# Kernel optimization log

Hardware: AMD Instinct MI355X
Metric: run time of the kernel (lower is better)

The kernel has to match this reference:

```python
import jax, jax.numpy as jnp
from jax import lax
import numpy as np

B, H, W, C = 4, 128, 128, 128   # C == d_route == n_heads, patch_len == H
OFFSET_RANGE = 5.0              # offset_range_factor == kernel == 5
SCALE = C ** -0.5               # self.scale_factor = d_route**-0.5
CYCLE = 168


def grid_sample_bilinear(img, grid):
    """torch.nn.functional.grid_sample(mode='bilinear', padding_mode='zeros', align_corners=False).
    img: (B,C,H,W); grid: (B,H,W,2) with (x,y) in [-1,1]."""
    Bn, Cn, Hn, Wn = img.shape
    xg = (grid[..., 0] + 1.0) * (Wn / 2.0) - 0.5
    yg = (grid[..., 1] + 1.0) * (Hn / 2.0) - 0.5
    x0 = jnp.floor(xg)
    y0 = jnp.floor(yg)
    img_flat = img.reshape(Bn, Cn, Hn * Wn)
    out = jnp.zeros_like(img)
    for xi in (x0, x0 + 1.0):
        for yi in (y0, y0 + 1.0):
            wgt = (1.0 - jnp.abs(xg - xi)) * (1.0 - jnp.abs(yg - yi))
            valid = (xi >= 0) & (xi <= Wn - 1) & (yi >= 0) & (yi <= Hn - 1)
            ix = jnp.clip(xi, 0, Wn - 1).astype(jnp.int32)
            iy = jnp.clip(yi, 0, Hn - 1).astype(jnp.int32)
            idx = (iy * Wn + ix).reshape(Bn, 1, -1)                      # (B,1,H*W)
            vals = jnp.take_along_axis(img_flat, idx, axis=2).reshape(Bn, Cn, Hn, Wn)
            out = out + vals * (wgt * valid.astype(img.dtype))[:, None, :, :]
    return out


def setup_inputs():
    key = jax.random.key(0)
    ks = jax.random.split(key, 12)
    s = C ** -0.5
    inp = {
        "x": jax.random.normal(ks[0], (B, H, W, C), dtype=jnp.float32),
        "cycle_index": jax.random.randint(ks[1], (B, 128), 0, CYCLE),  # dead path in cycle_mode='None'
        "Wq": jax.random.normal(ks[2], (C, C), dtype=jnp.float32) * s,
        "bq": jnp.zeros((C,), dtype=jnp.float32),
        "Wk": jax.random.normal(ks[3], (C, C), dtype=jnp.float32) * s,
        "bk": jnp.zeros((C,), dtype=jnp.float32),
        "Wv": jax.random.normal(ks[4], (C, C), dtype=jnp.float32) * s,
        "bv": jnp.zeros((C,), dtype=jnp.float32),
        "Wo": jax.random.normal(ks[5], (C, C), dtype=jnp.float32) * s,
        "bo": jnp.zeros((C,), dtype=jnp.float32),
        "Wc1": jax.random.normal(ks[6], (C, C, 5, 5), dtype=jnp.float32) * (1.0 / np.sqrt(C * 25)),
        "bc1": jnp.zeros((C,), dtype=jnp.float32),
        "Wc2": jax.random.normal(ks[7], (2, C), dtype=jnp.float32) * s,   # 1x1 conv, no bias
        "rel_bias": jax.random.normal(ks[8], (1, C, H, 1), dtype=jnp.float32) * 0.02,
    }
    return inp


def reference(x, cycle_index, Wq, bq, Wk, bk, Wv, bv, Wo, bo, Wc1, bc1, Wc2, rel_bias):
    Bn, Hn, Wn, Cn = x.shape
    xc = jnp.transpose(x, (0, 3, 1, 2))                                  # (B,C,H,W)
    # proj_q (1x1 conv) on x (cycle_mode='None')
    q = jnp.einsum('oc,bchw->bohw', Wq, xc) + bq[None, :, None, None]
    # proj_offset: 5x5 conv (pad 2) -> 1x1 conv to 2 channels, tanh * offset_range_factor
    c1 = lax.conv_general_dilated(q, Wc1, (1, 1), ((2, 2), (2, 2)),
                                  dimension_numbers=('NCHW', 'OIHW', 'NCHW')) + bc1[None, :, None, None]
    offset = jnp.tanh(jnp.einsum('oc,bchw->bohw', Wc2, c1)) * OFFSET_RANGE  # (B,2,H,W)
    # create_grid_like + normalize_grid (faithful, incl. x-coord normalized by H and vice versa)
    gx, gy = jnp.meshgrid(jnp.arange(Wn, dtype=x.dtype), jnp.arange(Hn, dtype=x.dtype), indexing='xy')
    grid = jnp.stack([gx, gy], axis=0)                                   # (2,H,W)
    vgrid = grid[None] + offset                                          # (B,2,H,W)
    gh = 2.0 * vgrid[:, 0] / max(Hn - 1, 1) - 1.0
    gw = 2.0 * vgrid[:, 1] / max(Wn - 1, 1) - 1.0
    sgrid = jnp.stack([gh, gw], axis=-1)                                 # (B,H,W,2) = (x,y) for grid_sample
    x_sampled = grid_sample_bilinear(xc, sgrid)                          # (B,C,H,W); n_groups=1 -> rearrange is identity
    k = (jnp.einsum('oc,bchw->bohw', Wk, x_sampled) + bk[None, :, None, None]).reshape(Bn * Cn, Hn, Wn)
    v = (jnp.einsum('oc,bchw->bohw', Wv, x_sampled) + bv[None, :, None, None] + rel_bias).reshape(Bn * Cn, Hn, Wn)
    qr = q.reshape(Bn * Cn, Hn, Wn)
    scores = jnp.einsum('bid,bjd->bij', qr, k) * SCALE                   # (B*C,H,H)
    attn = jax.nn.softmax(scores, axis=-1)
    out = jnp.einsum('bij,bjd->bid', attn, v)                            # (B*C,H,W)
    out = out.reshape(Bn, Hn, Wn, Cn)                                    # faithful raw reshape (as in original)
    return out @ Wo.T + bo
```

## Files before the change

kernel.cpp:

```cpp
#include <hip/hip_runtime.h>
#include <math.h>

#define IMG 16384

typedef short short8  __attribute__((ext_vector_type(8)));
typedef float floatx4 __attribute__((ext_vector_type(4)));

__device__ __forceinline__ float4 ld4(const float* p) {
    return *reinterpret_cast<const float4*>(p);
}
__device__ __forceinline__ short f2bf(float f) {
    union { float f; unsigned u; } v; v.f = f;
    unsigned r = v.u + 0x7fffu + ((v.u >> 16) & 1u);
    return (short)(r >> 16);
}
__device__ __forceinline__ float bf2f(short s) {
    union { unsigned u; float f; } v;
    v.u = ((unsigned)(unsigned short)s) << 16;
    return v.f;
}

__launch_bounds__(256)
__global__ void k_wprep(const float* __restrict__ Wc1, const float* __restrict__ Wc2,
                        const float* __restrict__ bc1, const float* __restrict__ Wq,
                        const float* __restrict__ bq,
                        float* __restrict__ W2, float* __restrict__ cst,
                        float* __restrict__ b_eff) {
    __shared__ float U[128];
    __shared__ float red[256];
    __shared__ float wc2[128];
    __shared__ float bql[128];
    const int tt = blockIdx.x;
    const int tch = tt / 25, tap = tt % 25;
    const int t = threadIdx.x;
    if (t < 128) { wc2[t] = Wc2[tch * 128 + t]; bql[t] = bq[t]; }
    __syncthreads();
    const int c = t & 127, half = t >> 7;
    float p = 0.f;
    for (int o = half * 64; o < half * 64 + 64; ++o)
        p += wc2[o] * Wc1[(o * 128 + c) * 25 + tap];
    red[half * 128 + c] = p;
    __syncthreads();
    if (t < 128) U[t] = red[t] + red[128 + t];
    __syncthreads();
    float p2 = 0.f;
    for (int cc = half * 64; cc < half * 64 + 64; ++cc)
        p2 += U[cc] * Wq[cc * 128 + c];
    red[half * 128 + c] = p2;
    __syncthreads();
    if (t < 128) W2[tt * 128 + t] = red[t] + red[128 + t];
    if (t < 128) red[t] = U[t] * bql[t];
    __syncthreads();
    if (t == 0) {
        float s = 0.f;
        for (int j = 0; j < 128; ++j) s += red[j];
        cst[tt] = s;
    }
    if (tap == 0) {
        __syncthreads();
        if (t < 128) red[t] = wc2[t] * bc1[t];
        __syncthreads();
        if (t == 0) {
            float s = 0.f;
            for (int j = 0; j < 128; ++j) s += red[j];
            b_eff[tch] = s;
        }
    }
}

__launch_bounds__(256)
__global__ void k_cvt(const float* __restrict__ x,
                      const float* __restrict__ Wq, const float* __restrict__ Wk,
                      const float* __restrict__ Wv, const float* __restrict__ Wo,
                      short* __restrict__ x_bf, short* __restrict__ wbf) {
    const int gid = blockIdx.x;
    if (gid < 4096) {
        int i = gid * 256 + threadIdx.x;
        const float* p = x + (size_t)i * 8;
        float4 a = ld4(p), b = ld4(p + 4);
        short8 o;
        o[0] = f2bf(a.x); o[1] = f2bf(a.y); o[2] = f2bf(a.z); o[3] = f2bf(a.w);
        o[4] = f2bf(b.x); o[5] = f2bf(b.y); o[6] = f2bf(b.z); o[7] = f2bf(b.w);
        *reinterpret_cast<short8*>(x_bf + (size_t)i * 8) = o;
    } else {
        int i = (gid - 4096) * 256 + threadIdx.x;
        int base = i * 8;
        int sel = base >> 14, off = base & 16383;
        const float* s = (sel == 0) ? Wq : (sel == 1) ? Wk : (sel == 2) ? Wv : Wo;
        float4 a = ld4(s + off), b = ld4(s + off + 4);
        short8 o;
        o[0] = f2bf(a.x); o[1] = f2bf(a.y); o[2] = f2bf(a.z); o[3] = f2bf(a.w);
        o[4] = f2bf(b.x); o[5] = f2bf(b.y); o[6] = f2bf(b.z); o[7] = f2bf(b.w);
        *reinterpret_cast<short8*>(wbf + base) = o;
    }
}

__launch_bounds__(256)
__global__ void k_off(const float* __restrict__ x, const float* __restrict__ W2,
                      const float* __restrict__ cst, float* __restrict__ P) {
    __shared__ float Wlds[128 * 68];
    __shared__ float Alds[32 * 68];
    const int t = threadIdx.x;
    const int pg = t & 15, og = t >> 4;
    const int p0 = blockIdx.x * 64;
    const int b = p0 >> 14, pix0 = p0 & (IMG - 1);

    for (int id = t; id < 128 * 64; id += 256) {
        int k = id >> 6, o = id & 63;
        Wlds[k * 68 + o] = (o < 50) ? W2[o * 128 + k] : 0.f;
    }
    float acc[4][4];
#pragma unroll
    for (int i = 0; i < 4; ++i)
#pragma unroll
        for (int j = 0; j < 4; ++j) acc[i][j] = 0.f;

    for (int kc = 0; kc < 128; kc += 32) {
        __syncthreads();
#pragma unroll
        for (int rep = 0; rep < 2; ++rep) {
            int id = rep * 256 + t;
            int m = id >> 3, k4 = (id & 7) * 4;
            float4 v = ld4(x + (size_t)(p0 + m) * 128 + kc + k4);
            Alds[(k4 + 0) * 68 + m] = v.x;
            Alds[(k4 + 1) * 68 + m] = v.y;
            Alds[(k4 + 2) * 68 + m] = v.z;
            Alds[(k4 + 3) * 68 + m] = v.w;
        }
        __syncthreads();
#pragma unroll
        for (int k = 0; k < 32; ++k) {
            float4 a = *reinterpret_cast<float4*>(&Alds[k * 68 + 4 * pg]);
            float4 wv = *reinterpret_cast<float4*>(&Wlds[(kc + k) * 68 + 4 * og]);
            float av[4] = {a.x, a.y, a.z, a.w};
            float wf[4] = {wv.x, wv.y, wv.z, wv.w};
#pragma unroll
            for (int i = 0; i < 4; ++i)
#pragma unroll
                for (int j = 0; j < 4; ++j)
                    acc[i][j] = fmaf(av[i], wf[j], acc[i][j]);
        }
    }
    __syncthreads();
#pragma unroll
    for (int j = 0; j < 4; ++j) {
        int o = 4 * og + j;
        float c = (o < 50) ? cst[o] : 0.f;
        *reinterpret_cast<float4*>(&Wlds[o * 68 + 4 * pg]) =
            make_float4(acc[0][j] + c, acc[1][j] + c, acc[2][j] + c, acc[3][j] + c);
    }
    __syncthreads();
    for (int id = t; id < 50 * 16; id += 256) {
        int o = id >> 4, px4 = (id & 15) * 4;
        float4 v = *reinterpret_cast<float4*>(&Wlds[o * 68 + px4]);
        *reinterpret_cast<float4*>(P + ((size_t)(b * 50 + o)) * IMG + pix0 + px4) = v;
    }
}

__launch_bounds__(256)
__global__ void k_fused(const float* __restrict__ P, const float* __restrict__ b_eff,
                        const short* __restrict__ x_bf, const short* __restrict__ wbf,
                        const float* __restrict__ bq, const float* __restrict__ bk,
                        const float* __restrict__ bv, const float* __restrict__ rel,
                        short* __restrict__ q_bf, short* __restrict__ k_bf,
                        short* __restrict__ v_bf) {
    __shared__ __align__(16) char smem[70656];
    float* rowsP  = (float*)smem;
    short* xrow   = (short*)smem;
    short* bufS   = (short*)smem;
    short* xsT    = (short*)(smem + 34816);
    float* offs_l = (float*)(smem + 69632);

    const int t = threadIdx.x;
    const int w = t >> 6, l = t & 63, l15 = l & 15, quad = l >> 4;
    const int mh = w >> 1, nh = w & 1;
    const int bh = blockIdx.x;
    const int b = bh >> 7, h = bh & 127;

    for (int id = t; id < 1600; id += 256) {
        int o = id >> 5, q4 = (id & 31) * 4;
        int di = (o % 25) / 5;
        int r = h + di - 2;
        float4 v = make_float4(0.f, 0.f, 0.f, 0.f);
        if (r >= 0 && r < 128)
            v = ld4(P + ((size_t)(b * 50 + o)) * IMG + r * 128 + q4);
        *reinterpret_cast<float4*>(&rowsP[o * 132 + q4]) = v;
    }
    __syncthreads();
    {
        int wp = t & 127, tc = t >> 7;
        float acc = 0.f;
#pragma unroll
        for (int di = 0; di < 5; ++di)
#pragma unroll
            for (int dj = 0; dj < 5; ++dj) {
                int wj = wp + dj - 2;
                if (wj >= 0 && wj < 128)
                    acc += rowsP[(tc * 25 + di * 5 + dj) * 132 + wj];
            }
        offs_l[tc * 128 + wp] = tanhf(acc + b_eff[tc]) * 5.0f;
    }
    __syncthreads();

    for (int id = t; id < 2048; id += 256) {
        int px = id >> 4, c8 = id & 15;
        *reinterpret_cast<short8*>(&xrow[px * 136 + c8 * 8]) =
            *reinterpret_cast<const short8*>(
                x_bf + (((size_t)(b * 128 + h)) * 128 + px) * 128 + c8 * 8);
    }
    for (int id = t; id < 2048; id += 256) {
        int px = id >> 4, c8 = id & 15;
        float ox = offs_l[px];
        float oy = offs_l[128 + px];
        float xg = ((float)px + ox) * (128.0f / 127.0f) - 0.5f;
        float yg = ((float)h  + oy) * (128.0f / 127.0f) - 0.5f;
        float x0f = floorf(xg), y0f = floorf(yg);
        float fx = xg - x0f, fy = yg - y0f;
        int x0 = (int)x0f, y0 = (int)y0f;
        float s[8];
#pragma unroll
        for (int r = 0; r < 8; ++r) s[r] = 0.f;
#pragma unroll
        for (int tap = 0; tap < 4; ++tap) {
            int xi = x0 + (tap & 1), yi = y0 + (tap >> 1);
            float wgt = ((tap & 1) ? fx : 1.f - fx) * ((tap >> 1) ? fy : 1.f - fy);
            if (xi >= 0 && xi < 128 && yi >= 0 && yi < 128) {
                short8 v = *reinterpret_cast<const short8*>(
                    x_bf + (((size_t)(b * 128 + yi)) * 128 + xi) * 128 + c8 * 8);
#pragma unroll
                for (int r = 0; r < 8; ++r) s[r] = fmaf(wgt, bf2f(v[r]), s[r]);
            }
        }
        short8 o;
#pragma unroll
        for (int r = 0; r < 8; ++r) o[r] = f2bf(s[r]);
        *reinterpret_cast<short8*>(&xsT[px * 136 + c8 * 8]) = o;
    }
    __syncthreads();

#pragma unroll
    for (int g = 0; g < 3; ++g) {
        const short* Asrc = (g == 0) ? xrow : xsT;
        const short* Wg   = wbf + g * 16384;
        const float* bias = (g == 0) ? bq : (g == 1) ? bk : bv;
        short* outg       = (g == 0) ? q_bf : (g == 1) ? k_bf : v_bf;

        floatx4 acc[4][4];
#pragma unroll
        for (int im = 0; im < 4; ++im)
#pragma unroll
            for (int in = 0; in < 4; ++in)
                acc[im][in] = (floatx4){0.f, 0.f, 0.f, 0.f};
#pragma unroll
        for (int kc = 0; kc < 128; kc += 32) {
            short8 af[4], bf_[4];
#pragma unroll
            for (int im = 0; im < 4; ++im)
                af[im] = *reinterpret_cast<const short8*>(
                    &Asrc[(mh * 64 + im * 16 + l15) * 136 + kc + quad * 8]);
#pragma unroll
            for (int in = 0; in < 4; ++in)
                bf_[in] = *reinterpret_cast<const short8*>(
                    Wg + (nh * 64 + in * 16 + l15) * 128 + kc + quad * 8);
#pragma unroll
            for (int im = 0; im < 4; ++im)
#pragma unroll
                for (int in = 0; in < 4; ++in)
                    acc[im][in] = __builtin_amdgcn_mfma_f32_16x16x32_bf16(
                        af[im], bf_[in], acc[im][in], 0, 0, 0);
        }
        float bb[4];
#pragma unroll
        for (int in = 0; in < 4; ++in) {
            int o = nh * 64 + in * 16 + l15;
            bb[in] = bias[o] + ((g == 2) ? rel[o * 128 + h] : 0.f);
        }
        __syncthreads();
#pragma unroll
        for (int im = 0; im < 4; ++im)
#pragma unroll
            for (int in = 0; in < 4; ++in) {
                int col = nh * 64 + in * 16 + l15;
#pragma unroll
                for (int r = 0; r < 4; ++r) {
                    int row = mh * 64 + im * 16 + quad * 4 + r;
                    bufS[col * 136 + row] = f2bf(acc[im][in][r] + bb[in]);
                }
            }
        __syncthreads();
        for (int id = t; id < 2048; id += 256) {
            int o = id >> 4, seg = id & 15;
            *reinterpret_cast<short8*>(
                outg + ((size_t)(b * 128 + o)) * IMG + h * 128 + seg * 8)
                = *reinterpret_cast<const short8*>(&bufS[o * 136 + seg * 8]);
        }
        __syncthreads();
    }
}

__launch_bounds__(256)
__global__ void k_attn3(const short* __restrict__ q_bf, const short* __restrict__ k_bf,
                        const short* __restrict__ v_bf, const short* __restrict__ WoB,
                        const float* __restrict__ bo, float* __restrict__ outp) {
    __shared__ __align__(16) short Pb[128 * 136];
    __shared__ __align__(16) short vT[128 * 136];
    __shared__ float redm[2 * 128];
    __shared__ float reds[2 * 128];

    const int t = threadIdx.x;
    const int w = t >> 6, l = t & 63, l15 = l & 15, quad = l >> 4;
    const int mh = w >> 1, nh = w & 1;
    const size_t hb = (size_t)blockIdx.x * IMG;
    const short* qp = q_bf + hb;
    const short* kp = k_bf + hb;
    const short* vp = v_bf + hb;

    for (int id = t; id < 2048; id += 256) {
        int j = id >> 4, seg = id & 15;
        short8 v8 = *reinterpret_cast<const short8*>(vp + j * 128 + seg * 8);
#pragma unroll
        for (int r = 0; r < 8; ++r)
            vT[(seg * 8 + r) * 136 + j] = v8[r];
    }

    floatx4 acc[4][4];
#pragma unroll
    for (int im = 0; im < 4; ++im)
#pragma unroll
        for (int in = 0; in < 4; ++in)
            acc[im][in] = (floatx4){0.f, 0.f, 0.f, 0.f};

#pragma unroll
    for (int kc = 0; kc < 128; kc += 32) {
        short8 af[4], bf_[4];
#pragma unroll
        for (int im = 0; im < 4; ++im)
            af[im] = *reinterpret_cast<const short8*>(
                qp + (mh * 64 + im * 16 + l15) * 128 + kc + quad * 8);
#pragma unroll
        for (int in = 0; in < 4; ++in)
            bf_[in] = *reinterpret_cast<const short8*>(
                kp + (nh * 64 + in * 16 + l15) * 128 + kc + quad * 8);
#pragma unroll
        for (int im = 0; im < 4; ++im)
#pragma unroll
            for (int in = 0; in < 4; ++in)
                acc[im][in] = __builtin_amdgcn_mfma_f32_16x16x32_bf16(
                    af[im], bf_[in], acc[im][in], 0, 0, 0);
    }

    const float scale = 0.08838834764831845f;
    float mloc[4][4];
#pragma unroll
    for (int im = 0; im < 4; ++im)
#pragma unroll
        for (int r = 0; r < 4; ++r) {
            float m = acc[im][0][r];
#pragma unroll
            for (int in = 1; in < 4; ++in) m = fmaxf(m, acc[im][in][r]);
            mloc[im][r] = m;
        }
#pragma unroll
    for (int mask = 1; mask < 16; mask <<= 1)
#pragma unroll
        for (int im = 0; im < 4; ++im)
#pragma unroll
            for (int r = 0; r < 4; ++r)
                mloc[im][r] = fmaxf(mloc[im][r], __shfl_xor(mloc[im][r], mask, 64));
    if (l15 == 0) {
#pragma unroll
        for (int im = 0; im < 4; ++im)
#pragma unroll
            for (int r = 0; r < 4; ++r)
                redm[nh * 128 + mh * 64 + im * 16 + quad * 4 + r] = mloc[im][r];
    }
    __syncthreads();
    float sloc[4][4];
#pragma unroll
    for (int im = 0; im < 4; ++im)
#pragma unroll
        for (int r = 0; r < 4; ++r) {
            int row = mh * 64 + im * 16 + quad * 4 + r;
            float m = fmaxf(redm[row], redm[128 + row]);
            float ss = 0.f;
#pragma unroll
            for (int in = 0; in < 4; ++in) {
                float e = __expf((acc[im][in][r] - m) * scale);
                acc[im][in][r] = e;
                ss += e;
            }
            sloc[im][r] = ss;
        }
#pragma unroll
    for (int mask = 1; mask < 16; mask <<= 1)
#pragma unroll
        for (int im = 0; im < 4; ++im)
#pragma unroll
            for (int r = 0; r < 4; ++r)
                sloc[im][r] += __shfl_xor(sloc[im][r], mask, 64);
    if (l15 == 0) {
#pragma unroll
        for (int im = 0; im < 4; ++im)
#pragma unroll
            for (int r = 0; r < 4; ++r)
                reds[nh * 128 + mh * 64 + im * 16 + quad * 4 + r] = sloc[im][r];
    }
    __syncthreads();
#pragma unroll
    for (int im = 0; im < 4; ++im)
#pragma unroll
        for (int r = 0; r < 4; ++r) {
            int row = mh * 64 + im * 16 + quad * 4 + r;
            float inv = 1.0f / (reds[row] + reds[128 + row]);
#pragma unroll
            for (int in = 0; in < 4; ++in) {
                int col = nh * 64 + in * 16 + l15;
                Pb[row * 136 + col] = f2bf(acc[im][in][r] * inv);
            }
        }
    __syncthreads();

#pragma unroll
    for (int im = 0; im < 4; ++im)
#pragma unroll
        for (int in = 0; in < 4; ++in)
            acc[im][in] = (floatx4){0.f, 0.f, 0.f, 0.f};
#pragma unroll
    for (int kc = 0; kc < 128; kc += 32) {
        short8 af[4], bf_[4];
#pragma unroll
        for (int im = 0; im < 4; ++im)
            af[im] = *reinterpret_cast<const short8*>(
                &Pb[(mh * 64 + im * 16 + l15) * 136 + kc + quad * 8]);
#pragma unroll
        for (int in = 0; in < 4; ++in)
            bf_[in] = *reinterpret_cast<const short8*>(
                &vT[(nh * 64 + in * 16 + l15) * 136 + kc + quad * 8]);
#pragma unroll
        for (int im = 0; im < 4; ++im)
#pragma unroll
            for (int in = 0; in < 4; ++in)
                acc[im][in] = __builtin_amdgcn_mfma_f32_16x16x32_bf16(
                    af[im], bf_[in], acc[im][in], 0, 0, 0);
    }
    __syncthreads();
#pragma unroll
    for (int im = 0; im < 4; ++im)
#pragma unroll
        for (int in = 0; in < 4; ++in) {
            int col = nh * 64 + in * 16 + l15;
#pragma unroll
            for (int r = 0; r < 4; ++r) {
                int row = mh * 64 + im * 16 + quad * 4 + r;
                Pb[row * 136 + col] = f2bf(acc[im][in][r]);
            }
        }
    __syncthreads();

    float bb[4];
#pragma unroll
    for (int in = 0; in < 4; ++in) bb[in] = bo[nh * 64 + in * 16 + l15];
#pragma unroll
    for (int im = 0; im < 4; ++im)
#pragma unroll
        for (int in = 0; in < 4; ++in)
            acc[im][in] = (floatx4){0.f, 0.f, 0.f, 0.f};
#pragma unroll
    for (int kc = 0; kc < 128; kc += 32) {
        short8 af[4], bf_[4];
#pragma unroll
        for (int im = 0; im < 4; ++im)
            af[im] = *reinterpret_cast<const short8*>(
                &Pb[(mh * 64 + im * 16 + l15) * 136 + kc + quad * 8]);
#pragma unroll
        for (int in = 0; in < 4; ++in)
            bf_[in] = *reinterpret_cast<const short8*>(
                WoB + (nh * 64 + in * 16 + l15) * 128 + kc + quad * 8);
#pragma unroll
        for (int im = 0; im < 4; ++im)
#pragma unroll
            for (int in = 0; in < 4; ++in)
                acc[im][in] = __builtin_amdgcn_mfma_f32_16x16x32_bf16(
                    af[im], bf_[in], acc[im][in], 0, 0, 0);
    }
#pragma unroll
    for (int im = 0; im < 4; ++im)
#pragma unroll
        for (int in = 0; in < 4; ++in) {
            int col = nh * 64 + in * 16 + l15;
#pragma unroll
            for (int r = 0; r < 4; ++r) {
                int row = mh * 64 + im * 16 + quad * 4 + r;
                outp[hb + (size_t)row * 128 + col] = acc[im][in][r] + bb[in];
            }
        }
}

extern "C" void kernel_launch(void* const* d_in, const int* in_sizes, int n_in,
                              void* d_out, int out_size, void* d_ws, size_t ws_size,
                              hipStream_t stream) {
    const float* x   = (const float*)d_in[0];
    const float* Wq  = (const float*)d_in[2];
    const float* bq  = (const float*)d_in[3];
    const float* Wk  = (const float*)d_in[4];
    const float* bk  = (const float*)d_in[5];
    const float* Wv  = (const float*)d_in[6];
    const float* bv  = (const float*)d_in[7];
    const float* Wo  = (const float*)d_in[8];
    const float* bo  = (const float*)d_in[9];
    const float* Wc1 = (const float*)d_in[10];
    const float* bc1 = (const float*)d_in[11];
    const float* Wc2 = (const float*)d_in[12];
    const float* rel = (const float*)d_in[13];

    char* wsb = (char*)d_ws;
    short* q_bf  = (short*)(wsb);
    short* k_bf  = (short*)(wsb + 1ull * 16777216);
    short* v_bf  = (short*)(wsb + 2ull * 16777216);
    short* x_bf  = (short*)(wsb + 3ull * 16777216);
    float* P     = (float*)(wsb + 4ull * 16777216);
    float* W2    = (float*)(wsb + 4ull * 16777216 + 13107200);
    float* cst   = W2 + 6400;
    float* b_eff = cst + 64;
    short* wbf   = (short*)(b_eff + 16);
    float* outp  = (float*)d_out;

    hipLaunchKernelGGL(k_cvt,   dim3(4128), dim3(256), 0, stream, x, Wq, Wk, Wv, Wo, x_bf, wbf);
    hipLaunchKernelGGL(k_wprep, dim3(50),   dim3(256), 0, stream, Wc1, Wc2, bc1, Wq, bq, W2, cst, b_eff);
    hipLaunchKernelGGL(k_off,   dim3(1024), dim3(256), 0, stream, x, W2, cst, P);
    hipLaunchKernelGGL(k_fused, dim3(512),  dim3(256), 0, stream, P, b_eff, x_bf, wbf,
                       bq, bk, bv, rel, q_bf, k_bf, v_bf);
    hipLaunchKernelGGL(k_attn3, dim3(512),  dim3(256), 0, stream, q_bf, k_bf, v_bf,
                       wbf + 49152, bo, outp);
}
```

Before: 223.4 us.

## Fold conversion kernel into wprep/offset kernels and restructure QKV projection

Removes the standalone fp32-to-bf16 conversion kernel. Weight conversion now runs in extra blocks of k_wprep, and x conversion happens inside k_off while it already loads x. The fused QKV kernel reads q-projection A operands straight from global x_bf instead of staging a row in LDS. It computes K and V in one pass sharing the sampled A fragments, and stores outputs directly as 4-wide bf16 writes instead of transposing through LDS. LDS is cut so two blocks fit per CU, at the cost of more register pressure and less coalesced global stores.

```diff
diff --git a/kernel.cpp b/kernel.cpp
--- a/kernel.cpp
+++ b/kernel.cpp
@@ -3,6 +3,7 @@
 
 #define IMG 16384
 
+typedef short short4v __attribute__((ext_vector_type(4)));
 typedef short short8  __attribute__((ext_vector_type(8)));
 typedef float floatx4 __attribute__((ext_vector_type(4)));
 
@@ -23,16 +24,29 @@
 __launch_bounds__(256)
 __global__ void k_wprep(const float* __restrict__ Wc1, const float* __restrict__ Wc2,
                         const float* __restrict__ bc1, const float* __restrict__ Wq,
-                        const float* __restrict__ bq,
+                        const float* __restrict__ bq, const float* __restrict__ Wk,
+                        const float* __restrict__ Wv, const float* __restrict__ Wo,
                         float* __restrict__ W2, float* __restrict__ cst,
-                        float* __restrict__ b_eff) {
+                        float* __restrict__ b_eff, short* __restrict__ wbf) {
+    const int t = threadIdx.x;
+    if (blockIdx.x >= 50) {
+        int i = (blockIdx.x - 50) * 256 + t;
+        int base = i * 8;
+        int sel = base >> 14, off = base & 16383;
+        const float* s = (sel == 0) ? Wq : (sel == 1) ? Wk : (sel == 2) ? Wv : Wo;
+        float4 a = ld4(s + off), b = ld4(s + off + 4);
+        short8 o;
+        o[0] = f2bf(a.x); o[1] = f2bf(a.y); o[2] = f2bf(a.z); o[3] = f2bf(a.w);
+        o[4] = f2bf(b.x); o[5] = f2bf(b.y); o[6] = f2bf(b.z); o[7] = f2bf(b.w);
+        *reinterpret_cast<short8*>(wbf + base) = o;
+        return;
+    }
     __shared__ float U[128];
     __shared__ float red[256];
     __shared__ float wc2[128];
     __shared__ float bql[128];
     const int tt = blockIdx.x;
     const int tch = tt / 25, tap = tt % 25;
-    const int t = threadIdx.x;
     if (t < 128) { wc2[t] = Wc2[tch * 128 + t]; bql[t] = bq[t]; }
     __syncthreads();
     const int c = t & 127, half = t >> 7;
@@ -69,35 +83,9 @@
 }
 
 __launch_bounds__(256)
-__global__ void k_cvt(const float* __restrict__ x,
-                      const float* __restrict__ Wq, const float* __restrict__ Wk,
-                      const float* __restrict__ Wv, const float* __restrict__ Wo,
-                      short* __restrict__ x_bf, short* __restrict__ wbf) {
-    const int gid = blockIdx.x;
-    if (gid < 4096) {
-        int i = gid * 256 + threadIdx.x;
-        const float* p = x + (size_t)i * 8;
-        float4 a = ld4(p), b = ld4(p + 4);
-        short8 o;
-        o[0] = f2bf(a.x); o[1] = f2bf(a.y); o[2] = f2bf(a.z); o[3] = f2bf(a.w);
-        o[4] = f2bf(b.x); o[5] = f2bf(b.y); o[6] = f2bf(b.z); o[7] = f2bf(b.w);
-        *reinterpret_cast<short8*>(x_bf + (size_t)i * 8) = o;
-    } else {
-        int i = (gid - 4096) * 256 + threadIdx.x;
-        int base = i * 8;
-        int sel = base >> 14, off = base & 16383;
-        const float* s = (sel == 0) ? Wq : (sel == 1) ? Wk : (sel == 2) ? Wv : Wo;
-        float4 a = ld4(s + off), b = ld4(s + off + 4);
-        short8 o;
-        o[0] = f2bf(a.x); o[1] = f2bf(a.y); o[2] = f2bf(a.z); o[3] = f2bf(a.w);
-        o[4] = f2bf(b.x); o[5] = f2bf(b.y); o[6] = f2bf(b.z); o[7] = f2bf(b.w);
-        *reinterpret_cast<short8*>(wbf + base) = o;
-    }
-}
-
-__launch_bounds__(256)
 __global__ void k_off(const float* __restrict__ x, const float* __restrict__ W2,
-                      const float* __restrict__ cst, float* __restrict__ P) {
+                      const float* __restrict__ cst, float* __restrict__ P,
+                      short* __restrict__ x_bf) {
     __shared__ float Wlds[128 * 68];
     __shared__ float Alds[32 * 68];
     const int t = threadIdx.x;
@@ -126,6 +114,8 @@
             Alds[(k4 + 1) * 68 + m] = v.y;
             Alds[(k4 + 2) * 68 + m] = v.z;
             Alds[(k4 + 3) * 68 + m] = v.w;
+            short4v s = {f2bf(v.x), f2bf(v.y), f2bf(v.z), f2bf(v.w)};
+            *reinterpret_cast<short4v*>(x_bf + (size_t)(p0 + m) * 128 + kc + k4) = s;
         }
         __syncthreads();
 #pragma unroll
@@ -157,19 +147,17 @@
     }
 }
 
-__launch_bounds__(256)
-__global__ void k_fused(const float* __restrict__ P, const float* __restrict__ b_eff,
-                        const short* __restrict__ x_bf, const short* __restrict__ wbf,
-                        const float* __restrict__ bq, const float* __restrict__ bk,
-                        const float* __restrict__ bv, const float* __restrict__ rel,
-                        short* __restrict__ q_bf, short* __restrict__ k_bf,
-                        short* __restrict__ v_bf) {
-    __shared__ __align__(16) char smem[70656];
+__launch_bounds__(256, 2)
+__global__ void k_fused2(const float* __restrict__ P, const float* __restrict__ b_eff,
+                         const short* __restrict__ x_bf, const short* __restrict__ wbf,
+                         const float* __restrict__ bq, const float* __restrict__ bk,
+                         const float* __restrict__ bv, const float* __restrict__ rel,
+                         short* __restrict__ q_bf, short* __restrict__ k_bf,
+                         short* __restrict__ v_bf) {
+    __shared__ __align__(16) char smem[62240];
     float* rowsP  = (float*)smem;
-    short* xrow   = (short*)smem;
-    short* bufS   = (short*)smem;
-    short* xsT    = (short*)(smem + 34816);
-    float* offs_l = (float*)(smem + 69632);
+    short* xsT    = (short*)(smem + 26400);
+    float* offs_l = (float*)(smem + 61216);
 
     const int t = threadIdx.x;
     const int w = t >> 6, l = t & 63, l15 = l & 15, quad = l >> 4;
@@ -202,12 +190,6 @@
     }
     __syncthreads();
 
-    for (int id = t; id < 2048; id += 256) {
-        int px = id >> 4, c8 = id & 15;
-        *reinterpret_cast<short8*>(&xrow[px * 136 + c8 * 8]) =
-            *reinterpret_cast<const short8*>(
-                x_bf + (((size_t)(b * 128 + h)) * 128 + px) * 128 + c8 * 8);
-    }
     for (int id = t; id < 2048; id += 256) {
         int px = id >> 4, c8 = id & 15;
         float ox = offs_l[px];
@@ -236,15 +218,9 @@
         for (int r = 0; r < 8; ++r) o[r] = f2bf(s[r]);
         *reinterpret_cast<short8*>(&xsT[px * 136 + c8 * 8]) = o;
     }
-    __syncthreads();
-
-#pragma unroll
-    for (int g = 0; g < 3; ++g) {
-        const short* Asrc = (g == 0) ? xrow : xsT;
-        const short* Wg   = wbf + g * 16384;
-        const float* bias = (g == 0) ? bq : (g == 1) ? bk : bv;
-        short* outg       = (g == 0) ? q_bf : (g == 1) ? k_bf : v_bf;
-
+
+    {
+        const short* xr = x_bf + ((size_t)(b * 128 + h)) * 128 * 128;
         floatx4 acc[4][4];
 #pragma unroll
         for (int im = 0; im < 4; ++im)
@@ -257,11 +233,11 @@
 #pragma unroll
             for (int im = 0; im < 4; ++im)
                 af[im] = *reinterpret_cast<const short8*>(
-                    &Asrc[(mh * 64 + im * 16 + l15) * 136 + kc + quad * 8]);
+                    xr + (mh * 64 + im * 16 + l15) * 128 + kc + quad * 8);
 #pragma unroll
             for (int in = 0; in < 4; ++in)
                 bf_[in] = *reinterpret_cast<const short8*>(
-                    Wg + (nh * 64 + in * 16 + l15) * 128 + kc + quad * 8);
+                    wbf + (nh * 64 + in * 16 + l15) * 128 + kc + quad * 8);
 #pragma unroll
             for (int im = 0; im < 4; ++im)
 #pragma unroll
@@ -269,32 +245,72 @@
                     acc[im][in] = __builtin_amdgcn_mfma_f32_16x16x32_bf16(
                         af[im], bf_[in], acc[im][in], 0, 0, 0);
         }
-        float bb[4];
 #pragma unroll
         for (int in = 0; in < 4; ++in) {
             int o = nh * 64 + in * 16 + l15;
-            bb[in] = bias[o] + ((g == 2) ? rel[o * 128 + h] : 0.f);
-        }
-        __syncthreads();
+            float bb = bq[o];
+#pragma unroll
+            for (int im = 0; im < 4; ++im) {
+                int px0 = mh * 64 + im * 16 + quad * 4;
+                short4v s = {f2bf(acc[im][in][0] + bb), f2bf(acc[im][in][1] + bb),
+                             f2bf(acc[im][in][2] + bb), f2bf(acc[im][in][3] + bb)};
+                *reinterpret_cast<short4v*>(
+                    q_bf + ((size_t)(b * 128 + o)) * IMG + h * 128 + px0) = s;
+            }
+        }
+    }
+    __syncthreads();
+
+    {
+        floatx4 ak[4][4], av[4][4];
 #pragma unroll
         for (int im = 0; im < 4; ++im)
 #pragma unroll
             for (int in = 0; in < 4; ++in) {
-                int col = nh * 64 + in * 16 + l15;
-#pragma unroll
-                for (int r = 0; r < 4; ++r) {
-                    int row = mh * 64 + im * 16 + quad * 4 + r;
-                    bufS[col * 136 + row] = f2bf(acc[im][in][r] + bb[in]);
+                ak[im][in] = (floatx4){0.f, 0.f, 0.f, 0.f};
+                av[im][in] = (floatx4){0.f, 0.f, 0.f, 0.f};
+            }
+#pragma unroll
+        for (int kc = 0; kc < 128; kc += 32) {
+            short8 af[4], bk_[4], bv_[4];
+#pragma unroll
+            for (int im = 0; im < 4; ++im)
+                af[im] = *reinterpret_cast<const short8*>(
+                    &xsT[(mh * 64 + im * 16 + l15) * 136 + kc + quad * 8]);
+#pragma unroll
+            for (int in = 0; in < 4; ++in) {
+                bk_[in] = *reinterpret_cast<const short8*>(
+                    wbf + 16384 + (nh * 64 + in * 16 + l15) * 128 + kc + quad * 8);
+                bv_[in] = *reinterpret_cast<const short8*>(
+                    wbf + 32768 + (nh * 64 + in * 16 + l15) * 128 + kc + quad * 8);
+            }
+#pragma unroll
+            for (int im = 0; im < 4; ++im)
+#pragma unroll
+                for (int in = 0; in < 4; ++in) {
+                    ak[im][in] = __builtin_amdgcn_mfma_f32_16x16x32_bf16(
+                        af[im], bk_[in], ak[im][in], 0, 0, 0);
+                    av[im][in] = __builtin_amdgcn_mfma_f32_16x16x32_bf16(
+                        af[im], bv_[in], av[im][in], 0, 0, 0);
                 }
-            }
-        __syncthreads();
-        for (int id = t; id < 2048; id += 256) {
-            int o = id >> 4, seg = id & 15;
-            *reinterpret_cast<short8*>(
-                outg + ((size_t)(b * 128 + o)) * IMG + h * 128 + seg * 8)
-                = *reinterpret_cast<const short8*>(&bufS[o * 136 + seg * 8]);
-        }
-        __syncthreads();
+        }
+#pragma unroll
+        for (int in = 0; in < 4; ++in) {
+            int o = nh * 64 + in * 16 + l15;
+            float bbk = bk[o];
+            float bbv = bv[o] + rel[o * 128 + h];
+#pragma unroll
+            for (int im = 0; im < 4; ++im) {
+                int px0 = mh * 64 + im * 16 + quad * 4;
+                size_t base = ((size_t)(b * 128 + o)) * IMG + h * 128 + px0;
+                short4v sk = {f2bf(ak[im][in][0] + bbk), f2bf(ak[im][in][1] + bbk),
+                              f2bf(ak[im][in][2] + bbk), f2bf(ak[im][in][3] + bbk)};
+                short4v sv = {f2bf(av[im][in][0] + bbv), f2bf(av[im][in][1] + bbv),
+                              f2bf(av[im][in][2] + bbv), f2bf(av[im][in][3] + bbv)};
+                *reinterpret_cast<short4v*>(k_bf + base) = sk;
+                *reinterpret_cast<short4v*>(v_bf + base) = sv;
+            }
+        }
     }
 }
 
@@ -525,11 +541,11 @@
     short* wbf   = (short*)(b_eff + 16);
     float* outp  = (float*)d_out;
 
-    hipLaunchKernelGGL(k_cvt,   dim3(4128), dim3(256), 0, stream, x, Wq, Wk, Wv, Wo, x_bf, wbf);
-    hipLaunchKernelGGL(k_wprep, dim3(50),   dim3(256), 0, stream, Wc1, Wc2, bc1, Wq, bq, W2, cst, b_eff);
-    hipLaunchKernelGGL(k_off,   dim3(1024), dim3(256), 0, stream, x, W2, cst, P);
-    hipLaunchKernelGGL(k_fused, dim3(512),  dim3(256), 0, stream, P, b_eff, x_bf, wbf,
+    hipLaunchKernelGGL(k_wprep,  dim3(82),   dim3(256), 0, stream, Wc1, Wc2, bc1, Wq, bq,
+                       Wk, Wv, Wo, W2, cst, b_eff, wbf);
+    hipLaunchKernelGGL(k_off,    dim3(1024), dim3(256), 0, stream, x, W2, cst, P, x_bf);
+    hipLaunchKernelGGL(k_fused2, dim3(512),  dim3(256), 0, stream, P, b_eff, x_bf, wbf,
                        bq, bk, bv, rel, q_bf, k_bf, v_bf);
-    hipLaunchKernelGGL(k_attn3, dim3(512),  dim3(256), 0, stream, q_bf, k_bf, v_bf,
+    hipLaunchKernelGGL(k_attn3,  dim3(512),  dim3(256), 0, stream, q_bf, k_bf, v_bf,
                        wbf + 49152, bo, outp);
 }
```

Result: slower. 236.5 us (+5.9%).
